# Kernel tuning notes

Measured on AMD Instinct MI355X. Metric: run time of the kernel, lower is better.

The kernel has to match this reference:

```python
import jax, jax.numpy as jnp
import numpy as np
import math

B, T, D = 4, 2048, 1024
H, KD, VD = 16, 64, 64


def setup_inputs() -> dict:
    key = jax.random.key(0)
    ks = jax.random.split(key, 10)
    s = 1.0 / math.sqrt(D)
    x = jax.random.normal(ks[0], (B, T, D), dtype=jnp.float32)
    # causal mask: True above the diagonal (positions to be masked out)
    mask = jnp.triu(jnp.ones((1, T, T), dtype=bool), k=1)
    Wq = jax.random.normal(ks[1], (H * KD, D), dtype=jnp.float32) * s
    bq = jnp.zeros((H * KD,), dtype=jnp.float32)
    Wk = jax.random.normal(ks[2], (H * KD, D), dtype=jnp.float32) * s
    bk = jnp.zeros((H * KD,), dtype=jnp.float32)
    Wv = jax.random.normal(ks[3], (H * VD, D), dtype=jnp.float32) * s
    bv = jnp.zeros((H * VD,), dtype=jnp.float32)
    Wo = jax.random.normal(ks[4], (D, H * VD), dtype=jnp.float32) * (1.0 / math.sqrt(H * VD))
    bo = jnp.zeros((D,), dtype=jnp.float32)
    return {"x": x, "mask": mask, "Wq": Wq, "bq": bq, "Wk": Wk, "bk": bk,
            "Wv": Wv, "bv": bv, "Wo": Wo, "bo": bo}


def reference(x, mask, Wq, bq, Wk, bk, Wv, bv, Wo, bo):
    b, t, d = x.shape
    # projections, reshaped to (b, h, t, head_dim)
    q = (x @ Wq.T + bq).reshape(b, t, H, KD).transpose(0, 2, 1, 3)
    k = (x @ Wk.T + bk).reshape(b, t, H, KD).transpose(0, 2, 1, 3)
    v = (x @ Wv.T + bv).reshape(b, t, H, VD).transpose(0, 2, 1, 3)
    scores = jnp.einsum('bhqd,bhkd->bhqk', q, k) / jnp.sqrt(jnp.float32(KD))
    # mask [1,T,T] broadcasts over batch and heads
    scores = jnp.where(mask[:, None, :, :], -jnp.inf, scores)
    attn = jax.nn.softmax(scores, axis=-1)
    out = jnp.einsum('bhqk,bhkd->bhqd', attn, v)  # (b,h,t,vd)
    out = out.transpose(0, 2, 1, 3).reshape(b, t, H * VD)
    return out @ Wo.T + bo
```

## Files before the change

### kernel.cpp

```cpp
#include <hip/hip_runtime.h>
#include <hip/hip_bf16.h>
#include <stdint.h>

#define B_ 4
#define T_ 2048
#define D_ 1024
#define H_ 16
#define HD_ 64

typedef __attribute__((ext_vector_type(8))) short bf16x8;
typedef __attribute__((ext_vector_type(4))) float f32x4;
typedef __attribute__((ext_vector_type(16))) float f32x16;

static __device__ __forceinline__ short f2bf(float f) {
    __hip_bfloat16 h = __float2bfloat16(f);
    short s;
    __builtin_memcpy(&s, &h, sizeof(short));
    return s;
}

static __device__ __forceinline__ void gload16(const void* g, void* l) {
    __builtin_amdgcn_global_load_lds((const __attribute__((address_space(1))) uint32_t*)g,
                                     (__attribute__((address_space(3))) uint32_t*)l,
                                     16, 0, 0);
}

static __device__ __forceinline__ unsigned cvtpk(float lo, float hi) {
    unsigned r;
    asm("v_cvt_pk_bf16_f32 %0, %1, %2" : "=v"(r) : "v"(lo), "v"(hi));
    return r;
}
static __device__ __forceinline__ void pl32swap(unsigned& a, unsigned& b) {
    asm("v_permlane32_swap_b32 %0, %1" : "+v"(a), "+v"(b));
}

__global__ __launch_bounds__(256) void cast_kernel(const float* __restrict__ src,
                                                   short* __restrict__ dst, int n) {
    int i = (blockIdx.x * 256 + threadIdx.x) * 4;
    if (i < n) {
        float4 v = *reinterpret_cast<const float4*>(src + i);
        short4 o;
        o.x = f2bf(v.x); o.y = f2bf(v.y); o.z = f2bf(v.z); o.w = f2bf(v.w);
        *reinterpret_cast<short4*>(dst + i) = o;
    }
}

__global__ __launch_bounds__(256) void cast_w_kernel(const float* __restrict__ wq,
                                                     const float* __restrict__ wk,
                                                     const float* __restrict__ wv,
                                                     const float* __restrict__ wo,
                                                     short* __restrict__ wqkv,
                                                     short* __restrict__ wob) {
    int wsel = blockIdx.x >> 10;
    int blk = blockIdx.x & 1023;
    const float* src = wsel == 0 ? wq : (wsel == 1 ? wk : (wsel == 2 ? wv : wo));
    short* dst = wsel == 3 ? wob : (wqkv + (size_t)wsel * 1024 * 1024);
    int i = (blk * 256 + threadIdx.x) * 4;
    float4 v = *reinterpret_cast<const float4*>(src + i);
    short4 o;
    o.x = f2bf(v.x); o.y = f2bf(v.y); o.z = f2bf(v.z); o.w = f2bf(v.w);
    *reinterpret_cast<short4*>(dst + i) = o;
}

template <int MODE>
__global__ __launch_bounds__(256) void gemm_kernel(
        const short* __restrict__ A, const short* __restrict__ Bw,
        const float* __restrict__ b0, const float* __restrict__ b1, const float* __restrict__ b2,
        short* __restrict__ q_out, short* __restrict__ k_out, short* __restrict__ v_out,
        float* __restrict__ f_out) {
    const int K = 1024;
    const int n0 = blockIdx.x * 128;
    const int m0 = blockIdx.y * 128;
    const int tid = threadIdx.x;
    const int wid = tid >> 6, lane = tid & 63, g = lane >> 4, c = lane & 15;
    const int wr = wid >> 1, wc = wid & 1;

    __shared__ __align__(16) short As[128 * 32];
    __shared__ __align__(16) short Bs[128 * 32];

    f32x4 acc[4][4] = {};

    for (int k0 = 0; k0 < K; k0 += 32) {
        #pragma unroll
        for (int r = 0; r < 2; ++r) {
            int ci = r * 256 + tid;
            int row = ci >> 2, cc = ci & 3;
            gload16(A + (size_t)(m0 + row) * K + k0 + cc * 8, As + ci * 8);
            gload16(Bw + (size_t)(n0 + row) * K + k0 + cc * 8, Bs + ci * 8);
        }
        __syncthreads();
        bf16x8 af[4], bfr[4];
        #pragma unroll
        for (int mt = 0; mt < 4; ++mt)
            af[mt] = *reinterpret_cast<const bf16x8*>(As + (wr * 64 + mt * 16 + c) * 32 + g * 8);
        #pragma unroll
        for (int nt = 0; nt < 4; ++nt)
            bfr[nt] = *reinterpret_cast<const bf16x8*>(Bs + (wc * 64 + nt * 16 + c) * 32 + g * 8);
        #pragma unroll
        for (int mt = 0; mt < 4; ++mt) {
            #pragma unroll
            for (int nt = 0; nt < 4; ++nt)
                acc[mt][nt] = __builtin_amdgcn_mfma_f32_16x16x32_bf16(af[mt], bfr[nt], acc[mt][nt], 0, 0, 0);
        }
        __syncthreads();
    }

    #pragma unroll
    for (int mt = 0; mt < 4; ++mt) {
        #pragma unroll
        for (int nt = 0; nt < 4; ++nt) {
            int n = n0 + wc * 64 + nt * 16 + c;
            if (MODE == 0) {
                int part = n >> 10, n1 = n & 1023;
                const float* bias = part == 0 ? b0 : (part == 1 ? b1 : b2);
                short* op = part == 0 ? q_out : (part == 1 ? k_out : v_out);
                int h = n1 >> 6, d = n1 & 63;
                float bb = bias[n1];
                #pragma unroll
                for (int r = 0; r < 4; ++r) {
                    int m = m0 + wr * 64 + mt * 16 + g * 4 + r;
                    int b = m >> 11, t = m & (T_ - 1);
                    op[((size_t)(b * H_ + h) * T_ + t) * HD_ + d] = f2bf(acc[mt][nt][r] + bb);
                }
            } else {
                float bb = b0[n];
                #pragma unroll
                for (int r = 0; r < 4; ++r) {
                    int m = m0 + wr * 64 + mt * 16 + g * 4 + r;
                    f_out[(size_t)m * 1024 + n] = acc[mt][nt][r] + bb;
                }
            }
        }
    }
}

__global__ __launch_bounds__(512) void attn_kernel(const short* __restrict__ q,
                                                   const short* __restrict__ k,
                                                   const short* __restrict__ v,
                                                   short* __restrict__ o) {
    const int h = blockIdx.y, b = blockIdx.z;
    const int bx = (int)gridDim.x - 1 - (int)blockIdx.x;
    const int q0b = bx * 256;
    const size_t base = ((size_t)(b * H_ + h)) * T_ * HD_;
    const int tid = threadIdx.x;
    const int wid = tid >> 6, lane = tid & 63;
    const int ql = lane & 31, hi = lane >> 5;
    const int q0w = q0b + wid * 32;
    const int qg = q0w + ql;
    const int xr = (ql & 7) << 3;

    __shared__ __align__(16) short lds[16384];

    const int kr = tid >> 3, ksl = tid & 7;
    const int kdoff = (ksl ^ (kr & 7)) << 3;
    const int vkey = tid & 63, vd0 = tid >> 6;

    bf16x8 qf[4];
    {
        const short* qrow = q + base + (size_t)qg * HD_ + hi * 8;
        #pragma unroll
        for (int st = 0; st < 4; ++st)
            qf[st] = *reinterpret_cast<const bf16x8*>(qrow + st * 16);
    }

    f32x16 oT0 = {}, oT1 = {};
    float m_r = -1e30f, l_r = 0.f;

    const int nT = (q0b + 256) >> 6;

    {
        gload16(k + base + (size_t)kr * HD_ + kdoff, lds + tid * 8);
        bf16x8 vv = *reinterpret_cast<const bf16x8*>(v + base + (size_t)vkey * HD_ + vd0 * 8);
        #pragma unroll
        for (int j = 0; j < 8; ++j)
            lds[8192 + (vd0 * 8 + j) * 64 + (vkey ^ (j << 3))] = vv[j];
    }
    __syncthreads();

    int buf = 0;
    for (int t0 = 0; t0 < nT; ++t0) {
        const int kv0 = t0 * 64;
        const bool pf = (t0 + 1 < nT);
        bf16x8 vnext;
        if (pf) {
            gload16(k + base + (size_t)(kv0 + 64 + kr) * HD_ + kdoff,
                    lds + (buf ^ 1) * 4096 + tid * 8);
            vnext = *reinterpret_cast<const bf16x8*>(v + base + (size_t)(kv0 + 64 + vkey) * HD_ + vd0 * 8);
        }

        if (kv0 <= q0w + 31) {
            const short* Kb = lds + buf * 4096;
            const short* Vb = lds + 8192 + buf * 4096;

            f32x16 s0 = {}, s1 = {};
            #pragma unroll
            for (int st = 0; st < 4; ++st) {
                int coff = (st * 16 + hi * 8) ^ xr;
                bf16x8 ka0 = *reinterpret_cast<const bf16x8*>(Kb + ql * 64 + coff);
                bf16x8 ka1 = *reinterpret_cast<const bf16x8*>(Kb + (32 + ql) * 64 + coff);
                s0 = __builtin_amdgcn_mfma_f32_32x32x16_bf16(ka0, qf[st], s0, 0, 0, 0);
                s1 = __builtin_amdgcn_mfma_f32_32x32x16_bf16(ka1, qf[st], s1, 0, 0, 0);
            }

            const float SC = 0.18033688f;
            if (kv0 + 63 <= q0w) {
                #pragma unroll
                for (int i = 0; i < 16; ++i) { s0[i] *= SC; s1[i] *= SC; }
            } else {
                #pragma unroll
                for (int i = 0; i < 16; ++i) {
                    int krow = (i & 3) + 8 * (i >> 2) + 4 * hi;
                    s0[i] = (kv0 + krow > qg) ? -1e30f : s0[i] * SC;
                    s1[i] = (kv0 + 32 + krow > qg) ? -1e30f : s1[i] * SC;
                }
            }

            float tm = s0[0];
            #pragma unroll
            for (int i = 1; i < 16; ++i) tm = fmaxf(tm, s0[i]);
            #pragma unroll
            for (int i = 0; i < 16; ++i) tm = fmaxf(tm, s1[i]);
            tm = fmaxf(tm, __shfl_xor(tm, 32, 64));
            float mn = fmaxf(m_r, tm);
            float al = exp2f(m_r - mn);
            m_r = mn;
            l_r *= al;
            #pragma unroll
            for (int i = 0; i < 16; ++i) { oT0[i] *= al; oT1[i] *= al; }
            float ts = 0.f;
            #pragma unroll
            for (int i = 0; i < 16; ++i) { s0[i] = exp2f(s0[i] - mn); ts += s0[i]; }
            #pragma unroll
            for (int i = 0; i < 16; ++i) { s1[i] = exp2f(s1[i] - mn); ts += s1[i]; }
            ts += __shfl_xor(ts, 32, 64);
            l_r += ts;

            unsigned c[16];
            #pragma unroll
            for (int i = 0; i < 8; ++i) c[i] = cvtpk(s0[2 * i], s0[2 * i + 1]);
            #pragma unroll
            for (int i = 0; i < 8; ++i) c[8 + i] = cvtpk(s1[2 * i], s1[2 * i + 1]);
            pl32swap(c[0], c[2]);  pl32swap(c[1], c[3]);
            pl32swap(c[4], c[6]);  pl32swap(c[5], c[7]);
            pl32swap(c[8], c[10]); pl32swap(c[9], c[11]);
            pl32swap(c[12], c[14]); pl32swap(c[13], c[15]);
            union { unsigned u[4]; bf16x8 v8; } pb[4];
            #pragma unroll
            for (int ksx = 0; ksx < 4; ++ksx) {
                #pragma unroll
                for (int j = 0; j < 4; ++j) pb[ksx].u[j] = c[ksx * 4 + j];
            }

            #pragma unroll
            for (int ksx = 0; ksx < 4; ++ksx) {
                int coff = (ksx * 16 + hi * 8) ^ xr;
                bf16x8 va0 = *reinterpret_cast<const bf16x8*>(Vb + ql * 64 + coff);
                bf16x8 va1 = *reinterpret_cast<const bf16x8*>(Vb + (32 + ql) * 64 + coff);
                oT0 = __builtin_amdgcn_mfma_f32_32x32x16_bf16(va0, pb[ksx].v8, oT0, 0, 0, 0);
                oT1 = __builtin_amdgcn_mfma_f32_32x32x16_bf16(va1, pb[ksx].v8, oT1, 0, 0, 0);
            }
        }

        if (pf) {
            #pragma unroll
            for (int j = 0; j < 8; ++j)
                lds[8192 + (buf ^ 1) * 4096 + (vd0 * 8 + j) * 64 + (vkey ^ (j << 3))] = vnext[j];
        }
        __syncthreads();
        buf ^= 1;
    }

    float inv = 1.f / l_r;
    const int row = wid * 32 + ql;
    #pragma unroll
    for (int i = 0; i < 16; ++i) {
        int d0 = (i & 3) + 8 * (i >> 2) + 4 * hi;
        lds[row * 64 + (d0 ^ xr)] = f2bf(oT0[i] * inv);
        lds[row * 64 + ((d0 + 32) ^ xr)] = f2bf(oT1[i] * inv);
    }
    __syncthreads();
    #pragma unroll
    for (int rr = 0; rr < 4; ++rr) {
        int orow = rr * 64 + (tid >> 3);
        int sl = tid & 7;
        bf16x8 val = *reinterpret_cast<const bf16x8*>(lds + orow * 64 + ((sl ^ (orow & 7)) << 3));
        *reinterpret_cast<bf16x8*>(o + ((size_t)(b * T_ + q0b + orow)) * D_ + h * HD_ + sl * 8) = val;
    }
}

extern "C" void kernel_launch(void* const* d_in, const int* in_sizes, int n_in,
                              void* d_out, int out_size, void* d_ws, size_t ws_size,
                              hipStream_t stream) {
    const float* x  = (const float*)d_in[0];
    const float* Wq = (const float*)d_in[2];
    const float* bq = (const float*)d_in[3];
    const float* Wk = (const float*)d_in[4];
    const float* bk = (const float*)d_in[5];
    const float* Wv = (const float*)d_in[6];
    const float* bv = (const float*)d_in[7];
    const float* Wo = (const float*)d_in[8];
    const float* bo = (const float*)d_in[9];
    float* out = (float*)d_out;

    const size_t NX = (size_t)B_ * T_ * D_;
    const size_t NW = (size_t)D_ * D_;

    short* ws   = (short*)d_ws;
    short* xb   = ws;
    short* ab   = ws;
    short* wqkv = xb + NX;
    short* wob  = wqkv + 3 * NW;
    short* qb   = wob + NW;
    short* kb   = qb + NX;
    short* vb   = kb + NX;

    cast_kernel<<<(int)(NX / 1024), 256, 0, stream>>>(x, xb, (int)NX);
    cast_w_kernel<<<4096, 256, 0, stream>>>(Wq, Wk, Wv, Wo, wqkv, wob);

    gemm_kernel<0><<<dim3(24, 64), 256, 0, stream>>>(xb, wqkv, bq, bk, bv, qb, kb, vb, nullptr);
    attn_kernel<<<dim3(T_ / 256, H_, B_), 512, 0, stream>>>(qb, kb, vb, ab);
    gemm_kernel<1><<<dim3(8, 64), 256, 0, stream>>>(ab, wob, bo, nullptr, nullptr, nullptr,
                                                    nullptr, nullptr, out);
}
```

Measured before the change: 359.2 us.

## Balance causal attention work by pairing short and long query tiles per block

Each attention block now handles two 128-row query tiles, blockIdx.x and its mirror, with 256 threads instead of one 256-row tile with 512 threads. This gives every block about the same causal workload, removing the imbalance where late-query blocks dominate the tail. It also adds s_setprio around the MFMA sections to favour matrix issue among waves. In exchange, each block has fewer waves to hide latency, and the K/V loads for the two phases are done separately.

```diff
diff --git a/kernel.cpp b/kernel.cpp
--- a/kernel.cpp
+++ b/kernel.cpp
@@ -134,157 +134,183 @@
     }
 }
 
-__global__ __launch_bounds__(512) void attn_kernel(const short* __restrict__ q,
+__global__ __launch_bounds__(256) void attn_kernel(const short* __restrict__ q,
                                                    const short* __restrict__ k,
                                                    const short* __restrict__ v,
                                                    short* __restrict__ o) {
     const int h = blockIdx.y, b = blockIdx.z;
-    const int bx = (int)gridDim.x - 1 - (int)blockIdx.x;
-    const int q0b = bx * 256;
     const size_t base = ((size_t)(b * H_ + h)) * T_ * HD_;
     const int tid = threadIdx.x;
     const int wid = tid >> 6, lane = tid & 63;
     const int ql = lane & 31, hi = lane >> 5;
-    const int q0w = q0b + wid * 32;
-    const int qg = q0w + ql;
     const int xr = (ql & 7) << 3;
 
     __shared__ __align__(16) short lds[16384];
 
-    const int kr = tid >> 3, ksl = tid & 7;
-    const int kdoff = (ksl ^ (kr & 7)) << 3;
-    const int vkey = tid & 63, vd0 = tid >> 6;
-
-    bf16x8 qf[4];
-    {
-        const short* qrow = q + base + (size_t)qg * HD_ + hi * 8;
-        #pragma unroll
-        for (int st = 0; st < 4; ++st)
-            qf[st] = *reinterpret_cast<const bf16x8*>(qrow + st * 16);
-    }
-
-    f32x16 oT0 = {}, oT1 = {};
-    float m_r = -1e30f, l_r = 0.f;
-
-    const int nT = (q0b + 256) >> 6;
-
-    {
-        gload16(k + base + (size_t)kr * HD_ + kdoff, lds + tid * 8);
-        bf16x8 vv = *reinterpret_cast<const bf16x8*>(v + base + (size_t)vkey * HD_ + vd0 * 8);
-        #pragma unroll
-        for (int j = 0; j < 8; ++j)
-            lds[8192 + (vd0 * 8 + j) * 64 + (vkey ^ (j << 3))] = vv[j];
-    }
-    __syncthreads();
-
-    int buf = 0;
-    for (int t0 = 0; t0 < nT; ++t0) {
-        const int kv0 = t0 * 64;
-        const bool pf = (t0 + 1 < nT);
-        bf16x8 vnext;
-        if (pf) {
-            gload16(k + base + (size_t)(kv0 + 64 + kr) * HD_ + kdoff,
-                    lds + (buf ^ 1) * 4096 + tid * 8);
-            vnext = *reinterpret_cast<const bf16x8*>(v + base + (size_t)(kv0 + 64 + vkey) * HD_ + vd0 * 8);
-        }
-
-        if (kv0 <= q0w + 31) {
-            const short* Kb = lds + buf * 4096;
-            const short* Vb = lds + 8192 + buf * 4096;
-
-            f32x16 s0 = {}, s1 = {};
+    const int krr = tid >> 3, ksl = tid & 7;
+    const int vkey = tid & 63, vd0b = tid >> 6;
+
+    const int nQJ = T_ / 128;
+    #pragma unroll 1
+    for (int ph = 0; ph < 2; ++ph) {
+        const int jj = ph == 0 ? (int)blockIdx.x : (nQJ - 1 - (int)blockIdx.x);
+        const int q0b = jj * 128;
+        const int q0w = q0b + wid * 32;
+        const int qg = q0w + ql;
+        const int nT = (q0b + 128) >> 6;
+
+        bf16x8 qf[4];
+        {
+            const short* qrow = q + base + (size_t)qg * HD_ + hi * 8;
             #pragma unroll
-            for (int st = 0; st < 4; ++st) {
-                int coff = (st * 16 + hi * 8) ^ xr;
-                bf16x8 ka0 = *reinterpret_cast<const bf16x8*>(Kb + ql * 64 + coff);
-                bf16x8 ka1 = *reinterpret_cast<const bf16x8*>(Kb + (32 + ql) * 64 + coff);
-                s0 = __builtin_amdgcn_mfma_f32_32x32x16_bf16(ka0, qf[st], s0, 0, 0, 0);
-                s1 = __builtin_amdgcn_mfma_f32_32x32x16_bf16(ka1, qf[st], s1, 0, 0, 0);
-            }
-
-            const float SC = 0.18033688f;
-            if (kv0 + 63 <= q0w) {
-                #pragma unroll
-                for (int i = 0; i < 16; ++i) { s0[i] *= SC; s1[i] *= SC; }
-            } else {
-                #pragma unroll
-                for (int i = 0; i < 16; ++i) {
-                    int krow = (i & 3) + 8 * (i >> 2) + 4 * hi;
-                    s0[i] = (kv0 + krow > qg) ? -1e30f : s0[i] * SC;
-                    s1[i] = (kv0 + 32 + krow > qg) ? -1e30f : s1[i] * SC;
-                }
-            }
-
-            float tm = s0[0];
-            #pragma unroll
-            for (int i = 1; i < 16; ++i) tm = fmaxf(tm, s0[i]);
-            #pragma unroll
-            for (int i = 0; i < 16; ++i) tm = fmaxf(tm, s1[i]);
-            tm = fmaxf(tm, __shfl_xor(tm, 32, 64));
-            float mn = fmaxf(m_r, tm);
-            float al = exp2f(m_r - mn);
-            m_r = mn;
-            l_r *= al;
-            #pragma unroll
-            for (int i = 0; i < 16; ++i) { oT0[i] *= al; oT1[i] *= al; }
-            float ts = 0.f;
-            #pragma unroll
-            for (int i = 0; i < 16; ++i) { s0[i] = exp2f(s0[i] - mn); ts += s0[i]; }
-            #pragma unroll
-            for (int i = 0; i < 16; ++i) { s1[i] = exp2f(s1[i] - mn); ts += s1[i]; }
-            ts += __shfl_xor(ts, 32, 64);
-            l_r += ts;
-
-            unsigned c[16];
-            #pragma unroll
-            for (int i = 0; i < 8; ++i) c[i] = cvtpk(s0[2 * i], s0[2 * i + 1]);
-            #pragma unroll
-            for (int i = 0; i < 8; ++i) c[8 + i] = cvtpk(s1[2 * i], s1[2 * i + 1]);
-            pl32swap(c[0], c[2]);  pl32swap(c[1], c[3]);
-            pl32swap(c[4], c[6]);  pl32swap(c[5], c[7]);
-            pl32swap(c[8], c[10]); pl32swap(c[9], c[11]);
-            pl32swap(c[12], c[14]); pl32swap(c[13], c[15]);
-            union { unsigned u[4]; bf16x8 v8; } pb[4];
-            #pragma unroll
-            for (int ksx = 0; ksx < 4; ++ksx) {
-                #pragma unroll
-                for (int j = 0; j < 4; ++j) pb[ksx].u[j] = c[ksx * 4 + j];
-            }
-
-            #pragma unroll
-            for (int ksx = 0; ksx < 4; ++ksx) {
-                int coff = (ksx * 16 + hi * 8) ^ xr;
-                bf16x8 va0 = *reinterpret_cast<const bf16x8*>(Vb + ql * 64 + coff);
-                bf16x8 va1 = *reinterpret_cast<const bf16x8*>(Vb + (32 + ql) * 64 + coff);
-                oT0 = __builtin_amdgcn_mfma_f32_32x32x16_bf16(va0, pb[ksx].v8, oT0, 0, 0, 0);
-                oT1 = __builtin_amdgcn_mfma_f32_32x32x16_bf16(va1, pb[ksx].v8, oT1, 0, 0, 0);
-            }
-        }
-
-        if (pf) {
+            for (int st = 0; st < 4; ++st)
+                qf[st] = *reinterpret_cast<const bf16x8*>(qrow + st * 16);
+        }
+
+        f32x16 oT0 = {}, oT1 = {};
+        float m_r = -1e30f, l_r = 0.f;
+
+        #pragma unroll
+        for (int r = 0; r < 2; ++r) {
+            int row = r * 32 + krr;
+            gload16(k + base + (size_t)row * HD_ + ((ksl ^ (row & 7)) << 3),
+                    lds + r * 2048 + tid * 8);
+        }
+        #pragma unroll
+        for (int cc = 0; cc < 2; ++cc) {
+            int vd0 = vd0b + cc * 4;
+            bf16x8 vv = *reinterpret_cast<const bf16x8*>(v + base + (size_t)vkey * HD_ + vd0 * 8);
             #pragma unroll
             for (int j = 0; j < 8; ++j)
-                lds[8192 + (buf ^ 1) * 4096 + (vd0 * 8 + j) * 64 + (vkey ^ (j << 3))] = vnext[j];
-        }
-        __syncthreads();
-        buf ^= 1;
-    }
-
-    float inv = 1.f / l_r;
-    const int row = wid * 32 + ql;
-    #pragma unroll
-    for (int i = 0; i < 16; ++i) {
-        int d0 = (i & 3) + 8 * (i >> 2) + 4 * hi;
-        lds[row * 64 + (d0 ^ xr)] = f2bf(oT0[i] * inv);
-        lds[row * 64 + ((d0 + 32) ^ xr)] = f2bf(oT1[i] * inv);
-    }
-    __syncthreads();
-    #pragma unroll
-    for (int rr = 0; rr < 4; ++rr) {
-        int orow = rr * 64 + (tid >> 3);
-        int sl = tid & 7;
-        bf16x8 val = *reinterpret_cast<const bf16x8*>(lds + orow * 64 + ((sl ^ (orow & 7)) << 3));
-        *reinterpret_cast<bf16x8*>(o + ((size_t)(b * T_ + q0b + orow)) * D_ + h * HD_ + sl * 8) = val;
+                lds[8192 + (vd0 * 8 + j) * 64 + (vkey ^ (j << 3))] = vv[j];
+        }
+        __syncthreads();
+
+        int buf = 0;
+        for (int t0 = 0; t0 < nT; ++t0) {
+            const int kv0 = t0 * 64;
+            const bool pf = (t0 + 1 < nT);
+            bf16x8 vnext[2];
+            if (pf) {
+                #pragma unroll
+                for (int r = 0; r < 2; ++r) {
+                    int row = r * 32 + krr;
+                    gload16(k + base + (size_t)(kv0 + 64 + row) * HD_ + ((ksl ^ (row & 7)) << 3),
+                            lds + (buf ^ 1) * 4096 + r * 2048 + tid * 8);
+                }
+                #pragma unroll
+                for (int cc = 0; cc < 2; ++cc)
+                    vnext[cc] = *reinterpret_cast<const bf16x8*>(
+                        v + base + (size_t)(kv0 + 64 + vkey) * HD_ + (vd0b + cc * 4) * 8);
+            }
+
+            if (kv0 <= q0w + 31) {
+                const short* Kb = lds + buf * 4096;
+                const short* Vb = lds + 8192 + buf * 4096;
+
+                f32x16 s0 = {}, s1 = {};
+                __builtin_amdgcn_s_setprio(1);
+                #pragma unroll
+                for (int st = 0; st < 4; ++st) {
+                    int coff = (st * 16 + hi * 8) ^ xr;
+                    bf16x8 ka0 = *reinterpret_cast<const bf16x8*>(Kb + ql * 64 + coff);
+                    bf16x8 ka1 = *reinterpret_cast<const bf16x8*>(Kb + (32 + ql) * 64 + coff);
+                    s0 = __builtin_amdgcn_mfma_f32_32x32x16_bf16(ka0, qf[st], s0, 0, 0, 0);
+                    s1 = __builtin_amdgcn_mfma_f32_32x32x16_bf16(ka1, qf[st], s1, 0, 0, 0);
+                }
+                __builtin_amdgcn_s_setprio(0);
+
+                const float SC = 0.18033688f;
+                if (kv0 + 63 <= q0w) {
+                    #pragma unroll
+                    for (int i = 0; i < 16; ++i) { s0[i] *= SC; s1[i] *= SC; }
+                } else {
+                    #pragma unroll
+                    for (int i = 0; i < 16; ++i) {
+                        int krow = (i & 3) + 8 * (i >> 2) + 4 * hi;
+                        s0[i] = (kv0 + krow > qg) ? -1e30f : s0[i] * SC;
+                        s1[i] = (kv0 + 32 + krow > qg) ? -1e30f : s1[i] * SC;
+                    }
+                }
+
+                float tm = s0[0];
+                #pragma unroll
+                for (int i = 1; i < 16; ++i) tm = fmaxf(tm, s0[i]);
+                #pragma unroll
+                for (int i = 0; i < 16; ++i) tm = fmaxf(tm, s1[i]);
+                tm = fmaxf(tm, __shfl_xor(tm, 32, 64));
+                float mn = fmaxf(m_r, tm);
+                float al = exp2f(m_r - mn);
+                m_r = mn;
+                l_r *= al;
+                #pragma unroll
+                for (int i = 0; i < 16; ++i) { oT0[i] *= al; oT1[i] *= al; }
+                float ts = 0.f;
+                #pragma unroll
+                for (int i = 0; i < 16; ++i) { s0[i] = exp2f(s0[i] - mn); ts += s0[i]; }
+                #pragma unroll
+                for (int i = 0; i < 16; ++i) { s1[i] = exp2f(s1[i] - mn); ts += s1[i]; }
+                ts += __shfl_xor(ts, 32, 64);
+                l_r += ts;
+
+                unsigned c[16];
+                #pragma unroll
+                for (int i = 0; i < 8; ++i) c[i] = cvtpk(s0[2 * i], s0[2 * i + 1]);
+                #pragma unroll
+                for (int i = 0; i < 8; ++i) c[8 + i] = cvtpk(s1[2 * i], s1[2 * i + 1]);
+                pl32swap(c[0], c[2]);   pl32swap(c[1], c[3]);
+                pl32swap(c[4], c[6]);   pl32swap(c[5], c[7]);
+                pl32swap(c[8], c[10]);  pl32swap(c[9], c[11]);
+                pl32swap(c[12], c[14]); pl32swap(c[13], c[15]);
+                union { unsigned u[4]; bf16x8 v8; } pb[4];
+                #pragma unroll
+                for (int ksx = 0; ksx < 4; ++ksx) {
+                    #pragma unroll
+                    for (int j = 0; j < 4; ++j) pb[ksx].u[j] = c[ksx * 4 + j];
+                }
+
+                __builtin_amdgcn_s_setprio(1);
+                #pragma unroll
+                for (int ksx = 0; ksx < 4; ++ksx) {
+                    int coff = (ksx * 16 + hi * 8) ^ xr;
+                    bf16x8 va0 = *reinterpret_cast<const bf16x8*>(Vb + ql * 64 + coff);
+                    bf16x8 va1 = *reinterpret_cast<const bf16x8*>(Vb + (32 + ql) * 64 + coff);
+                    oT0 = __builtin_amdgcn_mfma_f32_32x32x16_bf16(va0, pb[ksx].v8, oT0, 0, 0, 0);
+                    oT1 = __builtin_amdgcn_mfma_f32_32x32x16_bf16(va1, pb[ksx].v8, oT1, 0, 0, 0);
+                }
+                __builtin_amdgcn_s_setprio(0);
+            }
+
+            if (pf) {
+                #pragma unroll
+                for (int cc = 0; cc < 2; ++cc) {
+                    int vd0 = vd0b + cc * 4;
+                    #pragma unroll
+                    for (int j = 0; j < 8; ++j)
+                        lds[8192 + (buf ^ 1) * 4096 + (vd0 * 8 + j) * 64 + (vkey ^ (j << 3))] = vnext[cc][j];
+                }
+            }
+            __syncthreads();
+            buf ^= 1;
+        }
+
+        float inv = 1.f / l_r;
+        const int row = wid * 32 + ql;
+        #pragma unroll
+        for (int i = 0; i < 16; ++i) {
+            int d0 = (i & 3) + 8 * (i >> 2) + 4 * hi;
+            lds[8192 + row * 64 + (d0 ^ xr)] = f2bf(oT0[i] * inv);
+            lds[8192 + row * 64 + ((d0 + 32) ^ xr)] = f2bf(oT1[i] * inv);
+        }
+        __syncthreads();
+        #pragma unroll
+        for (int rr = 0; rr < 4; ++rr) {
+            int orow = rr * 32 + (tid >> 3);
+            int sl = tid & 7;
+            bf16x8 val = *reinterpret_cast<const bf16x8*>(lds + 8192 + orow * 64 + ((sl ^ (orow & 7)) << 3));
+            *reinterpret_cast<bf16x8*>(o + ((size_t)(b * T_ + q0b + orow)) * D_ + h * HD_ + sl * 8) = val;
+        }
+        __syncthreads();
     }
 }
 
@@ -318,7 +344,7 @@
     cast_w_kernel<<<4096, 256, 0, stream>>>(Wq, Wk, Wv, Wo, wqkv, wob);
 
     gemm_kernel<0><<<dim3(24, 64), 256, 0, stream>>>(xb, wqkv, bq, bk, bv, qb, kb, vb, nullptr);
-    attn_kernel<<<dim3(T_ / 256, H_, B_), 512, 0, stream>>>(qb, kb, vb, ab);
+    attn_kernel<<<dim3(T_ / 256, H_, B_), 256, 0, stream>>>(qb, kb, vb, ab);
     gemm_kernel<1><<<dim3(8, 64), 256, 0, stream>>>(ab, wob, bo, nullptr, nullptr, nullptr,
                                                     nullptr, nullptr, out);
 }
```

After: 351.1 us. 2.2% less time.
